# Kernel tuning notes

Measured on AMD Instinct MI355X. Metric: run time of the kernel, lower is better.

Reference implementation:

```python
import jax, jax.numpy as jnp
import numpy as np
import math

B, S, D, H = 4, 2048, 1024, 16
DK = D // H  # 64
THETA = 10000.0


def setup_inputs() -> dict:
    key = jax.random.key(0)
    ks = jax.random.split(key, 5)
    std = 0.02
    return {
        "x": jax.random.normal(ks[0], (B, S, D), dtype=jnp.float32),
        "Wq": jax.random.normal(ks[1], (D, D), dtype=jnp.float32) * std,
        "Wk": jax.random.normal(ks[2], (D, D), dtype=jnp.float32) * std,
        "Wv": jax.random.normal(ks[3], (D, D), dtype=jnp.float32) * std,
        "Wo": jax.random.normal(ks[4], (D, D), dtype=jnp.float32) * std / math.sqrt(2 * 12),
        "token_positions": jnp.arange(S, dtype=jnp.int32),
    }


def _rope(x, pos):
    # x: [B, H, S, DK]; pos: [S]. Interleaved-pair rotary embedding.
    inv_freq = THETA ** (-jnp.arange(0, DK, 2, dtype=jnp.float32) / DK)  # [DK/2]
    ang = pos.astype(jnp.float32)[:, None] * inv_freq[None, :]  # [S, DK/2]
    cos, sin = jnp.cos(ang), jnp.sin(ang)
    x1, x2 = x[..., 0::2], x[..., 1::2]  # [B, H, S, DK/2]
    r1 = x1 * cos - x2 * sin
    r2 = x1 * sin + x2 * cos
    return jnp.stack([r1, r2], axis=-1).reshape(x.shape)


def reference(x, Wq, Wk, Wv, Wo, token_positions):
    b, s, d = x.shape
    Q = x @ Wq
    K = x @ Wk
    V = x @ Wv
    # [B, S, D] -> [B, H, S, DK]
    def split(t):
        return t.reshape(b, s, H, DK).transpose(0, 2, 1, 3)
    Qh, Kh, Vh = split(Q), split(K), split(V)
    Qh = _rope(Qh, token_positions)
    Kh = _rope(Kh, token_positions)
    scores = jnp.einsum('bhqd,bhkd->bhqk', Qh, Kh) / math.sqrt(DK)
    causal = jnp.tril(jnp.ones((s, s), dtype=bool))
    scores = jnp.where(causal, scores, -jnp.inf)
    probs = jax.nn.softmax(scores, axis=-1)
    out = jnp.einsum('bhqk,bhkd->bhqd', probs, Vh)
    out = out.transpose(0, 2, 1, 3).reshape(b, s, d)
    return out @ Wo
```

## Files before the change

kernel.cpp:

```cpp
#include <hip/hip_runtime.h>
#include <hip/hip_bf16.h>

#define B_N 4
#define S_LEN 2048
#define D_MODEL 1024
#define N_HEAD 16
#define D_HEAD 64
#define M_ROWS (B_N * S_LEN)

typedef short bf16x8 __attribute__((ext_vector_type(8)));
typedef short bf16x4 __attribute__((ext_vector_type(4)));
typedef float f32x4 __attribute__((ext_vector_type(4)));

#if __has_builtin(__builtin_amdgcn_mfma_f32_16x16x16bf16_1k)
#define HAVE_MFMA16 1
#else
#define HAVE_MFMA16 0
#endif

__device__ __forceinline__ unsigned short f2bf(float f) {
  union { float f; unsigned int u; } v; v.f = f;
  unsigned int r = v.u + 0x7FFFu + ((v.u >> 16) & 1u);
  return (unsigned short)(r >> 16);
}
__device__ __forceinline__ float bf2f(unsigned short u) {
  union { unsigned int u; float f; } v; v.u = ((unsigned int)u) << 16;
  return v.f;
}
__device__ __forceinline__ unsigned int pkbf(float a, float b) {
  union { __hip_bfloat162 h; unsigned int u; } cv;
  cv.h = __float22bfloat162_rn(make_float2(a, b));
  return cv.u;
}
__device__ __forceinline__ bf16x8 ld8(const unsigned short* p) {
  return *reinterpret_cast<const bf16x8*>(p);
}
__device__ __forceinline__ bf16x4 ld4(const unsigned short* p) {
  return *reinterpret_cast<const bf16x4*>(p);
}
__device__ __forceinline__ void glds16(const unsigned short* g, unsigned short* l) {
  __builtin_amdgcn_global_load_lds(
      (const __attribute__((address_space(1))) unsigned int*)g,
      (__attribute__((address_space(3))) unsigned int*)l, 16, 0, 0);
}

__global__ __launch_bounds__(256) void rope_tab_k(const int* __restrict__ pos,
                                                  float2* __restrict__ tab) {
  const int idx = blockIdx.x * 256 + threadIdx.x;
  const int s = idx >> 5;
  const int i = idx & 31;
  const float inv = exp2f(-(float)i * 0.41524101186092029f);
  const float ang = (float)pos[s] * inv;
  tab[idx] = make_float2(cosf(ang), sinf(ang));
}

__global__ __launch_bounds__(256) void cast_k(const float* __restrict__ X,
                                              unsigned short* __restrict__ Y) {
  const size_t i = ((size_t)blockIdx.x * 256 + threadIdx.x) * 8;
  const float4 a = *reinterpret_cast<const float4*>(X + i);
  const float4 b = *reinterpret_cast<const float4*>(X + i + 4);
  union { unsigned int u[4]; uint4 v; } o;
  o.u[0] = pkbf(a.x, a.y); o.u[1] = pkbf(a.z, a.w);
  o.u[2] = pkbf(b.x, b.y); o.u[3] = pkbf(b.z, b.w);
  *reinterpret_cast<uint4*>(Y + i) = o.v;
}

__global__ __launch_bounds__(256) void wtrans_k(
    const float* __restrict__ W0, const float* __restrict__ W1,
    const float* __restrict__ W2, const float* __restrict__ W3,
    unsigned short* __restrict__ T0, unsigned short* __restrict__ T1,
    unsigned short* __restrict__ T2, unsigned short* __restrict__ T3) {
  const int z = blockIdx.z;
  const float* __restrict__ W = (z == 0) ? W0 : (z == 1) ? W1 : (z == 2) ? W2 : W3;
  unsigned short* __restrict__ T = (z == 0) ? T0 : (z == 1) ? T1 : (z == 2) ? T2 : T3;
  __shared__ __align__(16) unsigned short tile[64][72];
  const int kb = blockIdx.x * 64;
  const int nb = blockIdx.y * 64;
#pragma unroll
  for (int it = 0; it < 2; ++it) {
    const int chunk = it * 256 + threadIdx.x;
    const int r = chunk >> 3;
    const int c8 = (chunk & 7) * 8;
    const float* src = W + (size_t)(kb + r) * D_MODEL + nb + c8;
    const float4 a = *reinterpret_cast<const float4*>(src);
    const float4 b = *reinterpret_cast<const float4*>(src + 4);
    union { unsigned int u[4]; uint4 v; } o;
    o.u[0] = pkbf(a.x, a.y); o.u[1] = pkbf(a.z, a.w);
    o.u[2] = pkbf(b.x, b.y); o.u[3] = pkbf(b.z, b.w);
    *reinterpret_cast<uint4*>(&tile[r][c8]) = o.v;
  }
  __syncthreads();
#pragma unroll
  for (int it = 0; it < 2; ++it) {
    const int chunk = it * 256 + threadIdx.x;
    const int n = chunk >> 3;
    const int k8 = (chunk & 7) * 8;
    __align__(16) unsigned short vals[8];
#pragma unroll
    for (int j = 0; j < 8; ++j) vals[j] = tile[k8 + j][n];
    *reinterpret_cast<uint4*>(T + (size_t)(nb + n) * D_MODEL + kb + k8) =
        *reinterpret_cast<const uint4*>(vals);
  }
}

__global__ __launch_bounds__(256) void gemm2_k(
    const unsigned short* __restrict__ A, const unsigned short* __restrict__ W,
    unsigned short* __restrict__ Qo, unsigned short* __restrict__ Ko,
    unsigned short* __restrict__ VTo, float* __restrict__ OF,
    const float2* __restrict__ tab, const int mode) {
  __shared__ __align__(16) unsigned short smem[4][64][68];
  unsigned short* As = &smem[0][0][0];
  unsigned short* Bs = As + 128 * 32;

  const int tid = threadIdx.x;
  const int lane = tid & 63;
  const int w = tid >> 6;
  const int l15 = lane & 15;
  const int l4 = lane >> 4;

  const int row0 = blockIdx.x * 128;
  const int col0 = blockIdx.y * 128;

  const int srow = w * 32 + (lane >> 2);
  const int scol = (lane & 3) * 8;
  const unsigned short* ga = A + (size_t)(row0 + srow) * D_MODEL + scol;
  const unsigned short* gb = W + (size_t)(col0 + srow) * D_MODEL + scol;
  unsigned short* la = &As[(w * 32) * 32];
  unsigned short* lb = &Bs[(w * 32) * 32];

  const int wrow = (w & 1) * 64;
  const int wcol = (w >> 1) * 64;

  f32x4 acc[4][4];
  const f32x4 fz = {0.f, 0.f, 0.f, 0.f};
#pragma unroll
  for (int m = 0; m < 4; ++m)
#pragma unroll
    for (int n = 0; n < 4; ++n) acc[m][n] = fz;

  for (int kb = 0; kb < D_MODEL; kb += 32) {
    glds16(ga + kb, la);
    glds16(ga + 16 * D_MODEL + kb, la + 16 * 32);
    glds16(gb + kb, lb);
    glds16(gb + 16 * D_MODEL + kb, lb + 16 * 32);
    __syncthreads();
    bf16x8 af[4], bfr[4];
#pragma unroll
    for (int m = 0; m < 4; ++m) af[m] = ld8(&As[(wrow + m * 16 + l15) * 32 + l4 * 8]);
#pragma unroll
    for (int n = 0; n < 4; ++n) bfr[n] = ld8(&Bs[(wcol + n * 16 + l15) * 32 + l4 * 8]);
#pragma unroll
    for (int m = 0; m < 4; ++m)
#pragma unroll
      for (int n = 0; n < 4; ++n)
        acc[m][n] = __builtin_amdgcn_mfma_f32_16x16x32_bf16(af[m], bfr[n], acc[m][n], 0, 0, 0);
    __syncthreads();
  }

  if (mode == 1) {
#pragma unroll
    for (int n = 0; n < 4; ++n) {
      const int gcol = col0 + wcol + n * 16 + l15;
#pragma unroll
      for (int m = 0; m < 4; ++m)
#pragma unroll
        for (int r = 0; r < 4; ++r)
          OF[(size_t)(row0 + wrow + m * 16 + l4 * 4 + r) * D_MODEL + gcol] = acc[m][n][r];
    }
    return;
  }

  unsigned short (*T)[68] = (unsigned short(*)[68]) & smem[w];
  const bool isV = (col0 >= 2048);
  if (!isV) {
#pragma unroll
    for (int m = 0; m < 4; ++m)
#pragma unroll
      for (int n = 0; n < 4; ++n)
#pragma unroll
        for (int r = 0; r < 4; ++r)
          T[m * 16 + l4 * 4 + r][n * 16 + l15] = f2bf(acc[m][n][r]);
  } else {
#pragma unroll
    for (int m = 0; m < 4; ++m)
#pragma unroll
      for (int n = 0; n < 4; ++n)
#pragma unroll
        for (int r = 0; r < 4; ++r)
          T[n * 16 + l15][m * 16 + l4 * 4 + r] = f2bf(acc[m][n][r]);
  }

  const int lr = lane >> 3;
  const int lc = lane & 7;
  if (!isV) {
    const bool isQ = (col0 < 1024);
    unsigned short* O = isQ ? Qo : Ko;
    const float qs = isQ ? 0.18033688011112042f : 1.0f;
    const int cbase = (col0 & 1023) + wcol;
#pragma unroll
    for (int rg = 0; rg < 8; ++rg) {
      const int trow = rg * 8 + lr;
      const int grow = row0 + wrow + trow;
      const int s = grow & (S_LEN - 1);
      const bf16x8 vv = ld8(&T[trow][lc * 8]);
      const float4 tA = *reinterpret_cast<const float4*>(&tab[s * 32 + lc * 4]);
      const float4 tB = *reinterpret_cast<const float4*>(&tab[s * 32 + lc * 4 + 2]);
      float x[8];
#pragma unroll
      for (int j = 0; j < 8; ++j) x[j] = bf2f((unsigned short)vv[j]);
      union { unsigned int u[4]; uint4 v; } o;
      o.u[0] = pkbf((x[0] * tA.x - x[1] * tA.y) * qs, (x[0] * tA.y + x[1] * tA.x) * qs);
      o.u[1] = pkbf((x[2] * tA.z - x[3] * tA.w) * qs, (x[2] * tA.w + x[3] * tA.z) * qs);
      o.u[2] = pkbf((x[4] * tB.x - x[5] * tB.y) * qs, (x[4] * tB.y + x[5] * tB.x) * qs);
      o.u[3] = pkbf((x[6] * tB.z - x[7] * tB.w) * qs, (x[6] * tB.w + x[7] * tB.z) * qs);
      *reinterpret_cast<uint4*>(O + (size_t)grow * D_MODEL + cbase + lc * 8) = o.v;
    }
  } else {
    const int vc0 = (col0 - 2048) + wcol;
    const int h = vc0 >> 6;
    const int b = row0 >> 11;
    const int s0 = (row0 & (S_LEN - 1)) + wrow;
#pragma unroll
    for (int rg = 0; rg < 8; ++rg) {
      const int dk = rg * 8 + lr;
      const bf16x8 vv = ld8(&T[dk][lc * 8]);
      *reinterpret_cast<bf16x8*>(
          VTo + ((size_t)((b << 4) + h) * 64 + dk) * S_LEN + s0 + lc * 8) = vv;
    }
  }
}

__global__ __launch_bounds__(256) void attn5_k(
    const unsigned short* __restrict__ Q, const unsigned short* __restrict__ K,
    const unsigned short* __restrict__ VT, unsigned short* __restrict__ O) {
  const int pair = blockIdx.x;
  const int h = blockIdx.y;
  const int b = blockIdx.z;
  const int tid = threadIdx.x;
  const int w = tid >> 6;
  const int lane = tid & 63;
  const int l15 = lane & 15;
  const int l4 = lane >> 4;

  __shared__ __align__(16) unsigned short Ks[64][72];
  __shared__ __align__(16) unsigned short Vs[64][72];
#if !HAVE_MFMA16
  __shared__ __align__(16) unsigned short Ps[4][32][72];
#endif

  const f32x4 fz = {0.f, 0.f, 0.f, 0.f};
  const unsigned short* kbase = K + (size_t)b * S_LEN * D_MODEL + h * D_HEAD;
  const unsigned short* vbase = VT + (size_t)((b << 4) + h) * 64 * S_LEN;

  const int rr = tid >> 3;
  const int c8 = (tid & 7) * 8;

  for (int half = 0; half < 2; ++half) {
    const int qt = half ? (15 - pair) : pair;
    const int qb = qt * 128;
    const int qw0 = qb + w * 32;

    bf16x8 qf[2][2];
#pragma unroll
    for (int t = 0; t < 2; ++t)
#pragma unroll
      for (int kc = 0; kc < 2; ++kc)
        qf[t][kc] = ld8(Q + (size_t)(b * S_LEN + qw0 + t * 16 + l15) * D_MODEL +
                        h * D_HEAD + kc * 32 + l4 * 8);

    f32x4 o[4][2];
#pragma unroll
    for (int d = 0; d < 4; ++d)
#pragma unroll
      for (int t = 0; t < 2; ++t) o[d][t] = fz;
    float lsum[2] = {0.f, 0.f};

    const int nkt = qb / 64 + 2;
    for (int kt = 0; kt < nkt; ++kt) {
      const int kb0 = kt * 64;
#pragma unroll
      for (int it = 0; it < 2; ++it) {
        *reinterpret_cast<uint4*>(&Ks[rr + it * 32][c8]) =
            *reinterpret_cast<const uint4*>(kbase + (size_t)(kb0 + rr + it * 32) * D_MODEL + c8);
        *reinterpret_cast<uint4*>(&Vs[rr + it * 32][c8]) =
            *reinterpret_cast<const uint4*>(vbase + (size_t)(rr + it * 32) * S_LEN + kb0 + c8);
      }
      __syncthreads();

      if (kb0 <= qw0 + 31) {
        bf16x4 pf[2][4];
#pragma unroll
        for (int t = 0; t < 2; ++t) {
          f32x4 s[4];
#pragma unroll
          for (int n = 0; n < 4; ++n) {
            const bf16x8 kf0 = ld8(&Ks[n * 16 + l15][l4 * 8]);
            const bf16x8 kf1 = ld8(&Ks[n * 16 + l15][32 + l4 * 8]);
            f32x4 a0 = __builtin_amdgcn_mfma_f32_16x16x32_bf16(kf0, qf[t][0], fz, 0, 0, 0);
            s[n] = __builtin_amdgcn_mfma_f32_16x16x32_bf16(kf1, qf[t][1], a0, 0, 0, 0);
          }
          const bool full = (kb0 + 63 <= qw0 + t * 16);
          const int q = qw0 + t * 16 + l15;
          float su = lsum[t];
#pragma unroll
          for (int n = 0; n < 4; ++n) {
            float e[4];
            if (full) {
#pragma unroll
              for (int r = 0; r < 4; ++r) e[r] = exp2f(s[n][r]);
            } else {
#pragma unroll
              for (int r = 0; r < 4; ++r) {
                const int key = kb0 + n * 16 + l4 * 4 + r;
                const float v = exp2f(s[n][r]);
                e[r] = (key <= q) ? v : 0.f;
              }
            }
            su += (e[0] + e[1]) + (e[2] + e[3]);
            union { unsigned int u[2]; bf16x4 v; } pk;
            pk.u[0] = pkbf(e[0], e[1]);
            pk.u[1] = pkbf(e[2], e[3]);
            pf[t][n] = pk.v;
          }
          lsum[t] = su;
        }

#if HAVE_MFMA16
#pragma unroll
        for (int d = 0; d < 4; ++d) {
          bf16x4 vfc[4];
#pragma unroll
          for (int c = 0; c < 4; ++c) vfc[c] = ld4(&Vs[d * 16 + l15][c * 16 + l4 * 4]);
#pragma unroll
          for (int t = 0; t < 2; ++t)
#pragma unroll
            for (int c = 0; c < 4; ++c)
              o[d][t] = __builtin_amdgcn_mfma_f32_16x16x16bf16_1k(vfc[c], pf[t][c], o[d][t], 0, 0, 0);
        }
#else
#pragma unroll
        for (int t = 0; t < 2; ++t)
#pragma unroll
          for (int n = 0; n < 4; ++n)
            *reinterpret_cast<bf16x4*>(&Ps[w][t * 16 + l15][n * 16 + l4 * 4]) = pf[t][n];
        bf16x8 pfr[2][2], vf8[4][2];
#pragma unroll
        for (int t = 0; t < 2; ++t)
#pragma unroll
          for (int kc = 0; kc < 2; ++kc)
            pfr[t][kc] = ld8(&Ps[w][t * 16 + l15][kc * 32 + l4 * 8]);
#pragma unroll
        for (int d = 0; d < 4; ++d)
#pragma unroll
          for (int kc = 0; kc < 2; ++kc)
            vf8[d][kc] = ld8(&Vs[d * 16 + l15][kc * 32 + l4 * 8]);
#pragma unroll
        for (int d = 0; d < 4; ++d)
#pragma unroll
          for (int t = 0; t < 2; ++t) {
            o[d][t] = __builtin_amdgcn_mfma_f32_16x16x32_bf16(vf8[d][0], pfr[t][0], o[d][t], 0, 0, 0);
            o[d][t] = __builtin_amdgcn_mfma_f32_16x16x32_bf16(vf8[d][1], pfr[t][1], o[d][t], 0, 0, 0);
          }
#endif
      }
      __syncthreads();
    }

#pragma unroll
    for (int t = 0; t < 2; ++t) {
      float s = lsum[t];
      s += __shfl_xor(s, 16);
      s += __shfl_xor(s, 32);
      const float li = 1.0f / s;
      unsigned short* op = O + (size_t)(b * S_LEN + qw0 + t * 16 + l15) * D_MODEL +
                           h * D_HEAD + l4 * 4;
#pragma unroll
      for (int d = 0; d < 4; ++d) {
        union { unsigned int u[2]; uint2 v; } ov;
        ov.u[0] = pkbf(o[d][t][0] * li, o[d][t][1] * li);
        ov.u[1] = pkbf(o[d][t][2] * li, o[d][t][3] * li);
        *reinterpret_cast<uint2*>(op + d * 16) = ov.v;
      }
    }
  }
}

extern "C" void kernel_launch(void* const* d_in, const int* in_sizes, int n_in,
                              void* d_out, int out_size, void* d_ws, size_t ws_size,
                              hipStream_t stream) {
  const float* x  = (const float*)d_in[0];
  const float* Wq = (const float*)d_in[1];
  const float* Wk = (const float*)d_in[2];
  const float* Wv = (const float*)d_in[3];
  const float* Wo = (const float*)d_in[4];
  const int* pos  = (const int*)d_in[5];
  float* out = (float*)d_out;

  char* ws = (char*)d_ws;
  const size_t big = (size_t)M_ROWS * D_MODEL * 2;
  const size_t wsz = (size_t)D_MODEL * D_MODEL * 2;
  unsigned short* xb  = (unsigned short*)(ws + 0 * big);
  unsigned short* Qb  = (unsigned short*)(ws + 1 * big);
  unsigned short* Kb  = (unsigned short*)(ws + 2 * big);
  unsigned short* VT  = (unsigned short*)(ws + 3 * big);
  unsigned short* Wqkvt = (unsigned short*)(ws + 4 * big);
  unsigned short* Wot   = (unsigned short*)(ws + 4 * big + 3 * wsz);
  float2* tab = (float2*)d_out;

  rope_tab_k<<<dim3(S_LEN * 32 / 256), 256, 0, stream>>>(pos, tab);
  cast_k<<<dim3(M_ROWS * D_MODEL / 2048), 256, 0, stream>>>(x, xb);
  wtrans_k<<<dim3(16, 16, 4), 256, 0, stream>>>(
      Wq, Wk, Wv, Wo, Wqkvt, Wqkvt + (size_t)D_MODEL * D_MODEL,
      Wqkvt + 2 * (size_t)D_MODEL * D_MODEL, Wot);
  gemm2_k<<<dim3(M_ROWS / 128, 3 * D_MODEL / 128), 256, 0, stream>>>(
      xb, Wqkvt, Qb, Kb, VT, nullptr, tab, 0);
  attn5_k<<<dim3(8, N_HEAD, B_N), 256, 0, stream>>>(Qb, Kb, VT, Qb);
  gemm2_k<<<dim3(M_ROWS / 128, D_MODEL / 128), 256, 0, stream>>>(
      Qb, Wot, nullptr, nullptr, nullptr, out, nullptr, 1);
}
```

Measured before the change: 301.4 us.

## Split attention work across 8 waves of 16 query rows and prefetch K/V tiles

The attention kernel now launches 512 threads per block, so each wave owns 16 query rows instead of 32. This halves per-wave register state and gives finer-grained causal skipping. The next K/V tile is loaded into registers while the current tile is being stored to shared memory and processed, which overlaps global-load latency with compute. The cost is that each wave reads the shared K/V tiles for fewer query rows, which doubles LDS traffic per query. The larger block may also limit how many blocks fit on each CU.

```diff
diff --git a/kernel.cpp b/kernel.cpp
--- a/kernel.cpp
+++ b/kernel.cpp
@@ -230,7 +230,7 @@
   }
 }
 
-__global__ __launch_bounds__(256) void attn5_k(
+__global__ __launch_bounds__(512) void attn6_k(
     const unsigned short* __restrict__ Q, const unsigned short* __restrict__ K,
     const unsigned short* __restrict__ VT, unsigned short* __restrict__ O) {
   const int pair = blockIdx.x;
@@ -245,7 +245,7 @@
   __shared__ __align__(16) unsigned short Ks[64][72];
   __shared__ __align__(16) unsigned short Vs[64][72];
 #if !HAVE_MFMA16
-  __shared__ __align__(16) unsigned short Ps[4][32][72];
+  __shared__ __align__(16) unsigned short Ps[8][16][72];
 #endif
 
   const f32x4 fz = {0.f, 0.f, 0.f, 0.f};
@@ -258,72 +258,68 @@
   for (int half = 0; half < 2; ++half) {
     const int qt = half ? (15 - pair) : pair;
     const int qb = qt * 128;
-    const int qw0 = qb + w * 32;
-
-    bf16x8 qf[2][2];
-#pragma unroll
-    for (int t = 0; t < 2; ++t)
-#pragma unroll
-      for (int kc = 0; kc < 2; ++kc)
-        qf[t][kc] = ld8(Q + (size_t)(b * S_LEN + qw0 + t * 16 + l15) * D_MODEL +
-                        h * D_HEAD + kc * 32 + l4 * 8);
-
-    f32x4 o[4][2];
-#pragma unroll
-    for (int d = 0; d < 4; ++d)
-#pragma unroll
-      for (int t = 0; t < 2; ++t) o[d][t] = fz;
-    float lsum[2] = {0.f, 0.f};
+    const int qw0 = qb + w * 16;
+
+    bf16x8 qf[2];
+#pragma unroll
+    for (int kc = 0; kc < 2; ++kc)
+      qf[kc] = ld8(Q + (size_t)(b * S_LEN + qw0 + l15) * D_MODEL +
+                   h * D_HEAD + kc * 32 + l4 * 8);
+
+    f32x4 o[4];
+#pragma unroll
+    for (int d = 0; d < 4; ++d) o[d] = fz;
+    float lsum = 0.f;
 
     const int nkt = qb / 64 + 2;
+    uint4 kreg = *reinterpret_cast<const uint4*>(kbase + (size_t)rr * D_MODEL + c8);
+    uint4 vreg = *reinterpret_cast<const uint4*>(vbase + (size_t)rr * S_LEN + c8);
+
     for (int kt = 0; kt < nkt; ++kt) {
       const int kb0 = kt * 64;
-#pragma unroll
-      for (int it = 0; it < 2; ++it) {
-        *reinterpret_cast<uint4*>(&Ks[rr + it * 32][c8]) =
-            *reinterpret_cast<const uint4*>(kbase + (size_t)(kb0 + rr + it * 32) * D_MODEL + c8);
-        *reinterpret_cast<uint4*>(&Vs[rr + it * 32][c8]) =
-            *reinterpret_cast<const uint4*>(vbase + (size_t)(rr + it * 32) * S_LEN + kb0 + c8);
+      *reinterpret_cast<uint4*>(&Ks[rr][c8]) = kreg;
+      *reinterpret_cast<uint4*>(&Vs[rr][c8]) = vreg;
+      if (kt + 1 < nkt) {
+        const int nb0 = kb0 + 64;
+        kreg = *reinterpret_cast<const uint4*>(kbase + (size_t)(nb0 + rr) * D_MODEL + c8);
+        vreg = *reinterpret_cast<const uint4*>(vbase + (size_t)rr * S_LEN + nb0 + c8);
       }
       __syncthreads();
 
-      if (kb0 <= qw0 + 31) {
-        bf16x4 pf[2][4];
-#pragma unroll
-        for (int t = 0; t < 2; ++t) {
-          f32x4 s[4];
-#pragma unroll
-          for (int n = 0; n < 4; ++n) {
-            const bf16x8 kf0 = ld8(&Ks[n * 16 + l15][l4 * 8]);
-            const bf16x8 kf1 = ld8(&Ks[n * 16 + l15][32 + l4 * 8]);
-            f32x4 a0 = __builtin_amdgcn_mfma_f32_16x16x32_bf16(kf0, qf[t][0], fz, 0, 0, 0);
-            s[n] = __builtin_amdgcn_mfma_f32_16x16x32_bf16(kf1, qf[t][1], a0, 0, 0, 0);
+      if (kb0 <= qw0 + 15) {
+        f32x4 s[4];
+#pragma unroll
+        for (int n = 0; n < 4; ++n) {
+          const bf16x8 kf0 = ld8(&Ks[n * 16 + l15][l4 * 8]);
+          const bf16x8 kf1 = ld8(&Ks[n * 16 + l15][32 + l4 * 8]);
+          f32x4 a0 = __builtin_amdgcn_mfma_f32_16x16x32_bf16(kf0, qf[0], fz, 0, 0, 0);
+          s[n] = __builtin_amdgcn_mfma_f32_16x16x32_bf16(kf1, qf[1], a0, 0, 0, 0);
+        }
+        bf16x4 pf[4];
+        const bool full = (kb0 + 63 <= qw0);
+        const int q = qw0 + l15;
+        float su = lsum;
+#pragma unroll
+        for (int n = 0; n < 4; ++n) {
+          float e[4];
+          if (full) {
+#pragma unroll
+            for (int r = 0; r < 4; ++r) e[r] = exp2f(s[n][r]);
+          } else {
+#pragma unroll
+            for (int r = 0; r < 4; ++r) {
+              const int key = kb0 + n * 16 + l4 * 4 + r;
+              const float v = exp2f(s[n][r]);
+              e[r] = (key <= q) ? v : 0.f;
+            }
           }
-          const bool full = (kb0 + 63 <= qw0 + t * 16);
-          const int q = qw0 + t * 16 + l15;
-          float su = lsum[t];
-#pragma unroll
-          for (int n = 0; n < 4; ++n) {
-            float e[4];
-            if (full) {
-#pragma unroll
-              for (int r = 0; r < 4; ++r) e[r] = exp2f(s[n][r]);
-            } else {
-#pragma unroll
-              for (int r = 0; r < 4; ++r) {
-                const int key = kb0 + n * 16 + l4 * 4 + r;
-                const float v = exp2f(s[n][r]);
-                e[r] = (key <= q) ? v : 0.f;
-              }
-            }
-            su += (e[0] + e[1]) + (e[2] + e[3]);
-            union { unsigned int u[2]; bf16x4 v; } pk;
-            pk.u[0] = pkbf(e[0], e[1]);
-            pk.u[1] = pkbf(e[2], e[3]);
-            pf[t][n] = pk.v;
-          }
-          lsum[t] = su;
+          su += (e[0] + e[1]) + (e[2] + e[3]);
+          union { unsigned int u[2]; bf16x4 v; } pk;
+          pk.u[0] = pkbf(e[0], e[1]);
+          pk.u[1] = pkbf(e[2], e[3]);
+          pf[n] = pk.v;
         }
+        lsum = su;
 
 #if HAVE_MFMA16
 #pragma unroll
@@ -332,55 +328,41 @@
 #pragma unroll
           for (int c = 0; c < 4; ++c) vfc[c] = ld4(&Vs[d * 16 + l15][c * 16 + l4 * 4]);
 #pragma unroll
-          for (int t = 0; t < 2; ++t)
-#pragma unroll
-            for (int c = 0; c < 4; ++c)
-              o[d][t] = __builtin_amdgcn_mfma_f32_16x16x16bf16_1k(vfc[c], pf[t][c], o[d][t], 0, 0, 0);
+          for (int c = 0; c < 4; ++c)
+            o[d] = __builtin_amdgcn_mfma_f32_16x16x16bf16_1k(vfc[c], pf[c], o[d], 0, 0, 0);
         }
 #else
 #pragma unroll
-        for (int t = 0; t < 2; ++t)
-#pragma unroll
-          for (int n = 0; n < 4; ++n)
-            *reinterpret_cast<bf16x4*>(&Ps[w][t * 16 + l15][n * 16 + l4 * 4]) = pf[t][n];
-        bf16x8 pfr[2][2], vf8[4][2];
-#pragma unroll
-        for (int t = 0; t < 2; ++t)
-#pragma unroll
-          for (int kc = 0; kc < 2; ++kc)
-            pfr[t][kc] = ld8(&Ps[w][t * 16 + l15][kc * 32 + l4 * 8]);
-#pragma unroll
-        for (int d = 0; d < 4; ++d)
-#pragma unroll
-          for (int kc = 0; kc < 2; ++kc)
-            vf8[d][kc] = ld8(&Vs[d * 16 + l15][kc * 32 + l4 * 8]);
-#pragma unroll
-        for (int d = 0; d < 4; ++d)
-#pragma unroll
-          for (int t = 0; t < 2; ++t) {
-            o[d][t] = __builtin_amdgcn_mfma_f32_16x16x32_bf16(vf8[d][0], pfr[t][0], o[d][t], 0, 0, 0);
-            o[d][t] = __builtin_amdgcn_mfma_f32_16x16x32_bf16(vf8[d][1], pfr[t][1], o[d][t], 0, 0, 0);
-          }
+        for (int n = 0; n < 4; ++n)
+          *reinterpret_cast<bf16x4*>(&Ps[w][l15][n * 16 + l4 * 4]) = pf[n];
+        bf16x8 pfr[2];
+#pragma unroll
+        for (int kc = 0; kc < 2; ++kc)
+          pfr[kc] = ld8(&Ps[w][l15][kc * 32 + l4 * 8]);
+#pragma unroll
+        for (int d = 0; d < 4; ++d) {
+          const bf16x8 vf0 = ld8(&Vs[d * 16 + l15][l4 * 8]);
+          const bf16x8 vf1 = ld8(&Vs[d * 16 + l15][32 + l4 * 8]);
+          o[d] = __builtin_amdgcn_mfma_f32_16x16x32_bf16(vf0, pfr[0], o[d], 0, 0, 0);
+          o[d] = __builtin_amdgcn_mfma_f32_16x16x32_bf16(vf1, pfr[1], o[d], 0, 0, 0);
+        }
 #endif
       }
       __syncthreads();
     }
 
-#pragma unroll
-    for (int t = 0; t < 2; ++t) {
-      float s = lsum[t];
-      s += __shfl_xor(s, 16);
-      s += __shfl_xor(s, 32);
-      const float li = 1.0f / s;
-      unsigned short* op = O + (size_t)(b * S_LEN + qw0 + t * 16 + l15) * D_MODEL +
-                           h * D_HEAD + l4 * 4;
-#pragma unroll
-      for (int d = 0; d < 4; ++d) {
-        union { unsigned int u[2]; uint2 v; } ov;
-        ov.u[0] = pkbf(o[d][t][0] * li, o[d][t][1] * li);
-        ov.u[1] = pkbf(o[d][t][2] * li, o[d][t][3] * li);
-        *reinterpret_cast<uint2*>(op + d * 16) = ov.v;
-      }
+    float s = lsum;
+    s += __shfl_xor(s, 16);
+    s += __shfl_xor(s, 32);
+    const float li = 1.0f / s;
+    unsigned short* op = O + (size_t)(b * S_LEN + qw0 + l15) * D_MODEL +
+                         h * D_HEAD + l4 * 4;
+#pragma unroll
+    for (int d = 0; d < 4; ++d) {
+      union { unsigned int u[2]; uint2 v; } ov;
+      ov.u[0] = pkbf(o[d][0] * li, o[d][1] * li);
+      ov.u[1] = pkbf(o[d][2] * li, o[d][3] * li);
+      *reinterpret_cast<uint2*>(op + d * 16) = ov.v;
     }
   }
 }
@@ -414,7 +396,7 @@
       Wqkvt + 2 * (size_t)D_MODEL * D_MODEL, Wot);
   gemm2_k<<<dim3(M_ROWS / 128, 3 * D_MODEL / 128), 256, 0, stream>>>(
       xb, Wqkvt, Qb, Kb, VT, nullptr, tab, 0);
-  attn5_k<<<dim3(8, N_HEAD, B_N), 256, 0, stream>>>(Qb, Kb, VT, Qb);
+  attn6_k<<<dim3(8, N_HEAD, B_N), 512, 0, stream>>>(Qb, Kb, VT, Qb);
   gemm2_k<<<dim3(M_ROWS / 128, D_MODEL / 128), 256, 0, stream>>>(
       Qb, Wot, nullptr, nullptr, nullptr, out, nullptr, 1);
 }
```

Result: faster. 277.9 us (-7.8%).
